# Optimization experiments

Hardware: AMD Instinct MI355X
Metric: run time of the kernel (lower is better)

The kernel has to match this reference:

```python
import jax, jax.numpy as jnp
import numpy as np

N_NODES = 100000


def _spmm(edge_index, edge_weight, x):
    # out[i] = sum_j A[i, j] * x[j]; row=dst=edge_index[0], col=src=edge_index[1]
    dst, src = edge_index[0], edge_index[1]
    msgs = edge_weight[:, None] * x[src]  # [E, d]
    return jax.ops.segment_sum(msgs, dst, num_segments=N_NODES)


def setup_inputs() -> dict:
    key = jax.random.key(0)
    k1, k2, k3, k4 = jax.random.split(key, 4)
    N, E, D = N_NODES, 3200000, 64
    features = jax.random.normal(k1, (N, D), dtype=jnp.float32)
    edge_weight = jax.random.uniform(k2, (E,), dtype=jnp.float32)
    dst = jax.random.randint(k3, (E,), 0, N)
    src = jax.random.randint(k4, (E,), 0, N)
    edge_index = jnp.stack([dst, src]).astype(jnp.int64)
    return {"features": features, "edge_weight": edge_weight,
            "edge_index": edge_index, "degree": 2}


def reference(features, edge_weight, edge_index, degree):
    # SGC: features = adj @ features, repeated `degree` times (no learned params)
    x = features
    for _ in range(degree):
        x = _spmm(edge_index, edge_weight, x)
    return x
```

## Files before the change

kernel.cpp:

```cpp
#include <hip/hip_runtime.h>
#include <hip/hip_fp16.h>

#define N_NODES 100000
#define DFEAT 64
#define CH 8192
#define NBK 391
#define NPB 256
#define CAPB 9216

__device__ __forceinline__ int block_scan_excl_512(int v, int* sb, int tid, int* total)
{
    const int lane = tid & 63, wid = tid >> 6;
    int inc = v;
#pragma unroll
    for (int o = 1; o < 64; o <<= 1) {
        int t = __shfl_up(inc, o, 64);
        if (lane >= o) inc += t;
    }
    if (lane == 63) sb[wid] = inc;
    __syncthreads();
    if (wid == 0) {
        int wv = (lane < 8) ? sb[lane] : 0;
        int winc = wv;
#pragma unroll
        for (int o = 1; o < 8; o <<= 1) {
            int t = __shfl_up(winc, o, 64);
            if (lane >= o) winc += t;
        }
        if (lane < 8) sb[8 + lane] = winc - wv;
    }
    __syncthreads();
    *total = sb[15] + sb[7];
    return sb[8 + wid] + inc - v;
}

__global__ __launch_bounds__(512) void sort_chunks(
    const int* __restrict__ dst, const int* __restrict__ src,
    const float* __restrict__ w,
    unsigned* __restrict__ recs_g, unsigned char* __restrict__ dloc_g,
    int* __restrict__ off_T, int E, int nch,
    const float* __restrict__ feat_in, __half* __restrict__ feat_out, int n2)
{
    __shared__ int  hist[NBK + 1];
    __shared__ int  cursor[NBK];
    __shared__ int  sb[16];
    __shared__ unsigned      lrec[CH];
    __shared__ unsigned char ldl[CH];

    const int chunk = blockIdx.x;
    const int base  = chunk * CH;
    const int n     = min(CH, E - base);
    const int tid   = threadIdx.x;

    if (tid < NBK + 1) hist[tid] = 0;
    __syncthreads();

    for (int k = tid; k < n; k += 512) atomicAdd(&hist[dst[base + k] >> 8], 1);
    __syncthreads();

    int v = (tid < NBK) ? hist[tid] : 0;
    int tot;
    int excl = block_scan_excl_512(v, sb, tid, &tot);
    if (tid <= NBK) {
        off_T[(size_t)tid * nch + chunk] = base + excl;
        if (tid < NBK) cursor[tid] = excl;
    }
    __syncthreads();

    for (int k = tid; k < n; k += 512) {
        int d = dst[base + k];
        int pos = atomicAdd(&cursor[d >> 8], 1);
        unsigned wq = (unsigned)__float2int_rn(w[base + k] * 32768.0f);
        if (wq > 32767u) wq = 32767u;
        lrec[pos] = (unsigned)src[base + k] | (wq << 17);
        ldl[pos]  = (unsigned char)(d & 255);
    }
    __syncthreads();

    int4* rg = (int4*)(recs_g + base);
    const int4* rl = (const int4*)lrec;
    for (int k = tid; k < ((n + 3) >> 2); k += 512) rg[k] = rl[k];
    int4* dg = (int4*)(dloc_g + base);
    const int4* dl4 = (const int4*)ldl;
    for (int k = tid; k < ((n + 15) >> 4); k += 512) dg[k] = dl4[k];

    const int gstride = gridDim.x * 512;
    for (int i = blockIdx.x * 512 + tid; i < n2; i += gstride) {
        float2 f = ((const float2*)feat_in)[i];
        ((__half2*)feat_out)[i] = __floats2half2_rn(f.x, f.y);
    }
}

__global__ __launch_bounds__(512) void build_csr(
    const int* __restrict__ off_T, const unsigned* __restrict__ recs_g,
    const unsigned char* __restrict__ dloc_g,
    unsigned* __restrict__ edges_s, int* __restrict__ row_ptr,
    int nch, int E, int scan_const)
{
    __shared__ unsigned      lrecL[CAPB];
    __shared__ unsigned char dlocL[CAPB];
    __shared__ int gsrcL[512];
    __shared__ int lenL[512];
    __shared__ int ldstL[512];
    __shared__ int histL[NPB];
    __shared__ int cursorL[NPB];
    __shared__ int sb[16];

    const int b   = blockIdx.x;
    const int tid = threadIdx.x;

    int len = 0, a0v = 0;
    if (tid < nch) {
        int a0 = off_T[(size_t)b * nch + tid];
        int a1 = off_T[(size_t)(b + 1) * nch + tid];
        gsrcL[tid] = a0;
        a0v = a0;
        len = a1 - a0;
        lenL[tid] = len;
    }
    int rowsum;
    block_scan_excl_512(a0v, sb, tid, &rowsum);
    const int gb = rowsum - scan_const;

    int cnt;
    int dstoff = block_scan_excl_512(len, sb, tid, &cnt);
    if (tid < nch) ldstL[tid] = dstoff;
    if (tid < NPB) histL[tid] = 0;
    __syncthreads();

    const int grp = tid >> 4;
    const int gl  = tid & 15;
    for (int c = grp; c < nch; c += 32) {
        int s = gsrcL[c], d = ldstL[c], L = lenL[c];
        for (int k = gl; k < L; k += 16) {
            lrecL[d + k] = recs_g[s + k];
            dlocL[d + k] = dloc_g[s + k];
        }
    }
    __syncthreads();

    for (int k = tid; k < cnt; k += 512) atomicAdd(&histL[dlocL[k]], 1);
    __syncthreads();

    int hv = (tid < NPB) ? histL[tid] : 0;
    int htot;
    int hexcl = block_scan_excl_512(hv, sb, tid, &htot);
    if (tid < NPB) {
        int i = b * NPB + tid;
        if (i < N_NODES) row_ptr[i] = gb + hexcl;
        cursorL[tid] = gb + hexcl;
    }
    if (b == NBK - 1 && tid == 0) row_ptr[N_NODES] = E;
    __syncthreads();

    for (int k = tid; k < cnt; k += 512) {
        int pos = atomicAdd(&cursorL[dlocL[k]], 1);
        edges_s[pos] = lrecL[k];
    }
}

template <int OUT_FP16>
__global__ __launch_bounds__(256) void spmm_csr(
    const int* __restrict__ row_ptr,
    const unsigned* __restrict__ edges,
    const uint2* __restrict__ x4,
    void* __restrict__ outv)
{
    int node = __builtin_amdgcn_readfirstlane(blockIdx.x * 4 + (int)(threadIdx.x >> 6));
    if (node >= N_NODES) return;
    const int lane = threadIdx.x & 63;
    const int g    = lane >> 4;
    const int gl   = lane & 15;

    const int beg = row_ptr[node];
    const int end = row_ptr[node + 1];

    float a0 = 0.f, a1 = 0.f, a2 = 0.f, a3 = 0.f;
    int e0 = beg;
    const int nblk = (end - beg) >> 4;

#define ACC4(v, w) do {                                            \
        __half2 _h0 = *(__half2*)&(v).x;                           \
        __half2 _h1 = *(__half2*)&(v).y;                           \
        a0 += (w) * __low2float(_h0);  a1 += (w) * __high2float(_h0); \
        a2 += (w) * __low2float(_h1);  a3 += (w) * __high2float(_h1); \
    } while (0)

    if (nblk > 0) {
        unsigned n0 = edges[e0 +  0 + g];
        unsigned n1 = edges[e0 +  4 + g];
        unsigned n2 = edges[e0 +  8 + g];
        unsigned n3 = edges[e0 + 12 + g];
        e0 += 16;

        for (int b = 0; b < nblk; ++b) {
            uint2 v0 = x4[(size_t)(n0 & 0x1FFFF) * 16 + gl];
            uint2 v1 = x4[(size_t)(n1 & 0x1FFFF) * 16 + gl];
            uint2 v2 = x4[(size_t)(n2 & 0x1FFFF) * 16 + gl];
            uint2 v3 = x4[(size_t)(n3 & 0x1FFFF) * 16 + gl];

            float w0 = (float)(n0 >> 17), w1 = (float)(n1 >> 17);
            float w2 = (float)(n2 >> 17), w3 = (float)(n3 >> 17);

            if (b + 1 < nblk) {
                n0 = edges[e0 +  0 + g];
                n1 = edges[e0 +  4 + g];
                n2 = edges[e0 +  8 + g];
                n3 = edges[e0 + 12 + g];
                e0 += 16;
            }

            ACC4(v0, w0);
            ACC4(v1, w1);
            ACC4(v2, w2);
            ACC4(v3, w3);
        }
    }

    for (; e0 + 4 <= end; e0 += 4) {
        unsigned r = edges[e0 + g];
        uint2 v = x4[(size_t)(r & 0x1FFFF) * 16 + gl];
        float w = (float)(r >> 17);
        ACC4(v, w);
    }
    {
        int rem = end - e0;
        if (g < rem) {
            unsigned r = edges[e0 + g];
            uint2 v = x4[(size_t)(r & 0x1FFFF) * 16 + gl];
            float w = (float)(r >> 17);
            ACC4(v, w);
        }
    }
#undef ACC4

    a0 += __shfl_xor(a0, 16, 64);  a0 += __shfl_xor(a0, 32, 64);
    a1 += __shfl_xor(a1, 16, 64);  a1 += __shfl_xor(a1, 32, 64);
    a2 += __shfl_xor(a2, 16, 64);  a2 += __shfl_xor(a2, 32, 64);
    a3 += __shfl_xor(a3, 16, 64);  a3 += __shfl_xor(a3, 32, 64);

    if (g == 0) {
        const float k = 1.0f / 32768.0f;
        float s0 = a0 * k, s1 = a1 * k, s2 = a2 * k, s3 = a3 * k;
        if (OUT_FP16) {
            __half2 p0 = __floats2half2_rn(s0, s1);
            __half2 p1 = __floats2half2_rn(s2, s3);
            uint2 pv;
            pv.x = *(unsigned*)&p0;
            pv.y = *(unsigned*)&p1;
            ((uint2*)outv)[(size_t)node * 16 + gl] = pv;
        } else {
            ((float4*)outv)[(size_t)node * 16 + gl] = make_float4(s0, s1, s2, s3);
        }
    }
}

extern "C" void kernel_launch(void* const* d_in, const int* in_sizes, int n_in,
                              void* d_out, int out_size, void* d_ws, size_t ws_size,
                              hipStream_t stream) {
    const float* features = (const float*)d_in[0];
    const float* edge_w   = (const float*)d_in[1];
    const int*   edge_idx = (const int*)d_in[2];

    const int E = in_sizes[1];
    const int* dst = edge_idx;
    const int* src = edge_idx + E;

    const int nch = (E + CH - 1) / CH;

    char* ws = (char*)d_ws;
    unsigned*      recs_g  = (unsigned*)ws;      ws += (size_t)nch * CH * sizeof(unsigned);
    unsigned char* dloc_g  = (unsigned char*)ws; ws += (size_t)nch * CH;
    unsigned*      edges_s = (unsigned*)ws;      ws += (size_t)E * sizeof(unsigned);
    __half*        feat_h  = (__half*)ws;        ws += (size_t)N_NODES * DFEAT * sizeof(__half);
    int*           off_T   = (int*)ws;           ws += (size_t)(NBK + 1) * nch * sizeof(int);
    int*           row_ptr = (int*)ws;           ws += (size_t)(N_NODES + 1) * sizeof(int);

    __half* tmp_h = (__half*)recs_g;

    float* out = (float*)d_out;

    const int scan_const = (int)((long long)CH * (((long long)(nch - 1) * nch) / 2));

    const int n2 = N_NODES * DFEAT / 2;

    sort_chunks<<<nch, 512, 0, stream>>>(dst, src, edge_w, recs_g, dloc_g, off_T,
                                         E, nch, features, feat_h, n2);
    build_csr  <<<NBK, 512, 0, stream>>>(off_T, recs_g, dloc_g, edges_s, row_ptr,
                                         nch, E, scan_const);

    const int ngrid = (N_NODES + 3) / 4;
    spmm_csr<1><<<ngrid, 256, 0, stream>>>(row_ptr, edges_s, (const uint2*)feat_h, tmp_h);
    spmm_csr<0><<<ngrid, 256, 0, stream>>>(row_ptr, edges_s, (const uint2*)tmp_h, out);
}
```

Before: 270.3 us.

## Halve chunk and bucket sizes, use two-element scans and binary-search gather in CSR build

Chunk size drops to 4096 edges and destination buckets to 128 nodes, so there are twice as many buckets (782) and chunks. That gives more blocks and smaller shared-memory footprints per block in both the sort and the CSR-build kernels. Scans now handle two elements per thread, covering up to 1024 entries. The CSR gather now has each thread binary-search its source chunk instead of having 16-lane groups loop over chunks, which balances load when segments are short. The cost is off_T becoming larger, since the bucket count and chunk count both double, plus extra binary-search work per element.

```diff
diff --git a/kernel.cpp b/kernel.cpp
--- a/kernel.cpp
+++ b/kernel.cpp
@@ -3,15 +3,18 @@
 
 #define N_NODES 100000
 #define DFEAT 64
-#define CH 8192
-#define NBK 391
-#define NPB 256
-#define CAPB 9216
-
-__device__ __forceinline__ int block_scan_excl_512(int v, int* sb, int tid, int* total)
+#define CH 4096
+#define NBK 782
+#define NPB 128
+#define CAPB 4608
+
+__device__ __forceinline__ void scan2_1024(int v0, int v1, int* sb, int tid,
+                                           int* e0, int* e1, int* total)
 {
+    __syncthreads();
     const int lane = tid & 63, wid = tid >> 6;
-    int inc = v;
+    int s = v0 + v1;
+    int inc = s;
 #pragma unroll
     for (int o = 1; o < 64; o <<= 1) {
         int t = __shfl_up(inc, o, 64);
@@ -30,8 +33,10 @@
         if (lane < 8) sb[8 + lane] = winc - wv;
     }
     __syncthreads();
+    int base = sb[8 + wid] + inc - s;
+    *e0 = base;
+    *e1 = base + v0;
     *total = sb[15] + sb[7];
-    return sb[8 + wid] + inc - v;
 }
 
 __global__ __launch_bounds__(512) void sort_chunks(
@@ -52,28 +57,31 @@
     const int n     = min(CH, E - base);
     const int tid   = threadIdx.x;
 
-    if (tid < NBK + 1) hist[tid] = 0;
-    __syncthreads();
-
-    for (int k = tid; k < n; k += 512) atomicAdd(&hist[dst[base + k] >> 8], 1);
-    __syncthreads();
-
-    int v = (tid < NBK) ? hist[tid] : 0;
-    int tot;
-    int excl = block_scan_excl_512(v, sb, tid, &tot);
-    if (tid <= NBK) {
-        off_T[(size_t)tid * nch + chunk] = base + excl;
-        if (tid < NBK) cursor[tid] = excl;
-    }
+    for (int i = tid; i < NBK + 1; i += 512) hist[i] = 0;
+    __syncthreads();
+
+    for (int k = tid; k < n; k += 512) atomicAdd(&hist[dst[base + k] >> 7], 1);
+
+    const int i0 = 2 * tid, i1 = 2 * tid + 1;
+    int v0 = 0, v1 = 0;
+    __syncthreads();
+    v0 = (i0 < NBK) ? hist[i0] : 0;
+    v1 = (i1 < NBK) ? hist[i1] : 0;
+    int e0, e1, tot;
+    scan2_1024(v0, v1, sb, tid, &e0, &e1, &tot);
+    if (i0 <= NBK) off_T[(size_t)i0 * nch + chunk] = base + e0;
+    if (i1 <= NBK) off_T[(size_t)i1 * nch + chunk] = base + e1;
+    if (i0 < NBK) cursor[i0] = e0;
+    if (i1 < NBK) cursor[i1] = e1;
     __syncthreads();
 
     for (int k = tid; k < n; k += 512) {
         int d = dst[base + k];
-        int pos = atomicAdd(&cursor[d >> 8], 1);
+        int pos = atomicAdd(&cursor[d >> 7], 1);
         unsigned wq = (unsigned)__float2int_rn(w[base + k] * 32768.0f);
         if (wq > 32767u) wq = 32767u;
         lrec[pos] = (unsigned)src[base + k] | (wq << 17);
-        ldl[pos]  = (unsigned char)(d & 255);
+        ldl[pos]  = (unsigned char)(d & 127);
     }
     __syncthreads();
 
@@ -99,9 +107,8 @@
 {
     __shared__ unsigned      lrecL[CAPB];
     __shared__ unsigned char dlocL[CAPB];
-    __shared__ int gsrcL[512];
-    __shared__ int lenL[512];
-    __shared__ int ldstL[512];
+    __shared__ int gsrcL[NBK];
+    __shared__ int ldstL[NBK];
     __shared__ int histL[NPB];
     __shared__ int cursorL[NPB];
     __shared__ int sb[16];
@@ -109,51 +116,71 @@
     const int b   = blockIdx.x;
     const int tid = threadIdx.x;
 
-    int len = 0, a0v = 0;
-    if (tid < nch) {
-        int a0 = off_T[(size_t)b * nch + tid];
-        int a1 = off_T[(size_t)(b + 1) * nch + tid];
-        gsrcL[tid] = a0;
-        a0v = a0;
-        len = a1 - a0;
-        lenL[tid] = len;
-    }
-    int rowsum;
-    block_scan_excl_512(a0v, sb, tid, &rowsum);
+    const int c0 = 2 * tid, c1 = c0 + 1;
+    int a00 = 0, a01 = 0, l0 = 0, l1 = 0;
+    if (c0 < nch) {
+        a00 = off_T[(size_t)b * nch + c0];
+        int a1 = off_T[(size_t)(b + 1) * nch + c0];
+        gsrcL[c0] = a00;
+        l0 = a1 - a00;
+    }
+    if (c1 < nch) {
+        a01 = off_T[(size_t)b * nch + c1];
+        int a1 = off_T[(size_t)(b + 1) * nch + c1];
+        gsrcL[c1] = a01;
+        l1 = a1 - a01;
+    }
+
+    int ra, rb_, rowsum;
+    scan2_1024(a00, a01, sb, tid, &ra, &rb_, &rowsum);
     const int gb = rowsum - scan_const;
 
-    int cnt;
-    int dstoff = block_scan_excl_512(len, sb, tid, &cnt);
-    if (tid < nch) ldstL[tid] = dstoff;
+    int d0, d1, cnt;
+    scan2_1024(l0, l1, sb, tid, &d0, &d1, &cnt);
+    if (c0 < nch) ldstL[c0] = d0;
+    if (c1 < nch) ldstL[c1] = d1;
     if (tid < NPB) histL[tid] = 0;
     __syncthreads();
 
-    const int grp = tid >> 4;
-    const int gl  = tid & 15;
-    for (int c = grp; c < nch; c += 32) {
-        int s = gsrcL[c], d = ldstL[c], L = lenL[c];
-        for (int k = gl; k < L; k += 16) {
-            lrecL[d + k] = recs_g[s + k];
-            dlocL[d + k] = dloc_g[s + k];
-        }
-    }
-    __syncthreads();
-
-    for (int k = tid; k < cnt; k += 512) atomicAdd(&histL[dlocL[k]], 1);
-    __syncthreads();
-
-    int hv = (tid < NPB) ? histL[tid] : 0;
-    int htot;
-    int hexcl = block_scan_excl_512(hv, sb, tid, &htot);
-    if (tid < NPB) {
-        int i = b * NPB + tid;
-        if (i < N_NODES) row_ptr[i] = gb + hexcl;
-        cursorL[tid] = gb + hexcl;
+    const int cntC = min(cnt, CAPB);
+
+#pragma unroll
+    for (int j = 0; j < (CAPB + 511) / 512; ++j) {
+        int k = tid + j * 512;
+        if (k < cntC) {
+            int lo = 0, hi = nch;
+            while (hi - lo > 1) {
+                int mid = (lo + hi) >> 1;
+                if (ldstL[mid] <= k) lo = mid; else hi = mid;
+            }
+            int sp = gsrcL[lo] + (k - ldstL[lo]);
+            lrecL[k] = recs_g[sp];
+            dlocL[k] = dloc_g[sp];
+        }
+    }
+    __syncthreads();
+
+    for (int k = tid; k < cntC; k += 512) atomicAdd(&histL[dlocL[k]], 1);
+    __syncthreads();
+
+    int h0 = (2 * tid < NPB) ? histL[2 * tid] : 0;
+    int h1 = (2 * tid + 1 < NPB) ? histL[2 * tid + 1] : 0;
+    int he0, he1, htot;
+    scan2_1024(h0, h1, sb, tid, &he0, &he1, &htot);
+    if (2 * tid < NPB) {
+        int i = b * NPB + 2 * tid;
+        if (i < N_NODES) row_ptr[i] = gb + he0;
+        cursorL[2 * tid] = gb + he0;
+    }
+    if (2 * tid + 1 < NPB) {
+        int i = b * NPB + 2 * tid + 1;
+        if (i < N_NODES) row_ptr[i] = gb + he1;
+        cursorL[2 * tid + 1] = gb + he1;
     }
     if (b == NBK - 1 && tid == 0) row_ptr[N_NODES] = E;
     __syncthreads();
 
-    for (int k = tid; k < cnt; k += 512) {
+    for (int k = tid; k < cntC; k += 512) {
         int pos = atomicAdd(&cursorL[dlocL[k]], 1);
         edges_s[pos] = lrecL[k];
     }
```

Result: faster. 262.9 us (-2.7%).
